# Optimization experiments

Measured on AMD Instinct MI355X. Metric: run time of the kernel, lower is better.

Reference implementation:

```python
import jax, jax.numpy as jnp
import numpy as np

HEADS = 4
CH = 64  # hidden_channels (per-head out channels)
N_INT = 50000
N_LANE = 400000
E_PO = 400000
E_ADJ = 200000


def setup_inputs() -> dict:
    key = jax.random.key(0)
    ks = iter(jax.random.split(key, 32))
    rn = lambda shape, s=0.1: jax.random.normal(next(ks), shape, dtype=jnp.float32) * s
    inp = {
        'x_int': rn((N_INT, 16), 1.0),
        'x_lane': rn((N_LANE, 12), 1.0),
        'h0': jnp.zeros((N_INT, CH), jnp.float32),
        'enc_int_W': rn((16, CH)), 'enc_int_b': jnp.zeros((CH,), jnp.float32),
        'enc_lane_W': rn((12, CH)), 'enc_lane_b': jnp.zeros((CH,), jnp.float32),
        'Wsrc_po': rn((CH, HEADS * CH)), 'Wdst_po': rn((CH, HEADS * CH)),
        'att_src_po': rn((HEADS, CH)), 'att_dst_po': rn((HEADS, CH)),
        'bias_po': jnp.zeros((HEADS * CH,), jnp.float32),
        'Wsrc_adj': rn((CH, HEADS * CH)), 'Wdst_adj': rn((CH, HEADS * CH)),
        'att_src_adj': rn((HEADS, CH)), 'att_dst_adj': rn((HEADS, CH)),
        'bias_adj': jnp.zeros((HEADS * CH,), jnp.float32),
        'gru_W_ih': rn((3 * CH, HEADS * CH)), 'gru_W_hh': rn((3 * CH, CH)),
        'gru_b_ih': jnp.zeros((3 * CH,), jnp.float32), 'gru_b_hh': jnp.zeros((3 * CH,), jnp.float32),
        'W_pi': rn((CH, 8)), 'b_pi': jnp.zeros((8,), jnp.float32),
        'W_v': rn((CH, 1)), 'b_v': jnp.zeros((1,), jnp.float32),
        'src_po': jax.random.randint(next(ks), (E_PO,), 0, N_LANE),
        'dst_po': jax.random.randint(next(ks), (E_PO,), 0, N_INT),
        'src_adj': jax.random.randint(next(ks), (E_ADJ,), 0, N_INT),
        'dst_adj': jax.random.randint(next(ks), (E_ADJ,), 0, N_INT),
    }
    return inp


def gat_conv(x_src, x_dst, src, dst, Wsrc, Wdst, a_src, a_dst, bias, n_dst):
    # PyG GATConv (bipartite, concat=True, no self loops), negative_slope=0.2
    hs = (x_src @ Wsrc).reshape(-1, HEADS, CH)  # [Ns,H,C]
    hd = (x_dst @ Wdst).reshape(-1, HEADS, CH)  # [Nd,H,C]
    a_s = jnp.einsum('nhc,hc->nh', hs, a_src)   # [Ns,H]
    a_d = jnp.einsum('nhc,hc->nh', hd, a_dst)   # [Nd,H]
    alpha = jax.nn.leaky_relu(a_s[src] + a_d[dst], 0.2)        # [E,H]
    amax = jax.ops.segment_max(alpha, dst, num_segments=n_dst)  # [Nd,H]
    ex = jnp.exp(alpha - amax[dst])
    den = jax.ops.segment_sum(ex, dst, num_segments=n_dst)
    w = ex / den[dst]                                           # [E,H] softmax per dst
    msg = hs[src] * w[:, :, None]                               # [E,H,C]
    out = jax.ops.segment_sum(msg, dst, num_segments=n_dst)     # [Nd,H,C]
    return out.reshape(n_dst, HEADS * CH) + bias


def gru_cell(x, h, W_ih, W_hh, b_ih, b_hh):
    gi = x @ W_ih.T + b_ih
    gh = h @ W_hh.T + b_hh
    i_r, i_z, i_n = jnp.split(gi, 3, axis=1)
    h_r, h_z, h_n = jnp.split(gh, 3, axis=1)
    r = jax.nn.sigmoid(i_r + h_r)
    z = jax.nn.sigmoid(i_z + h_z)
    n = jnp.tanh(i_n + r * h_n)
    return (1.0 - z) * n + z * h


def reference(x_int, x_lane, h0, enc_int_W, enc_int_b, enc_lane_W, enc_lane_b,
              Wsrc_po, Wdst_po, att_src_po, att_dst_po, bias_po,
              Wsrc_adj, Wdst_adj, att_src_adj, att_dst_adj, bias_adj,
              gru_W_ih, gru_W_hh, gru_b_ih, gru_b_hh,
              W_pi, b_pi, W_v, b_v,
              src_po, dst_po, src_adj, dst_adj):
    # per-type encoders + ReLU
    e_int = jax.nn.relu(x_int @ enc_int_W + enc_int_b)    # [N_int,CH]
    e_lane = jax.nn.relu(x_lane @ enc_lane_W + enc_lane_b)  # [N_lane,CH]
    # HeteroConv aggr='sum' over relations targeting 'intersection'
    o_po = gat_conv(e_lane, e_int, src_po, dst_po, Wsrc_po, Wdst_po,
                    att_src_po, att_dst_po, bias_po, N_INT)
    o_adj = gat_conv(e_int, e_int, src_adj, dst_adj, Wsrc_adj, Wdst_adj,
                     att_src_adj, att_dst_adj, bias_adj, N_INT)
    inter = jax.nn.relu(o_po + o_adj)  # dropout = identity (deterministic eval)
    h_new = gru_cell(inter, h0, gru_W_ih, gru_W_hh, gru_b_ih, gru_b_hh)
    logits = h_new @ W_pi + b_pi
    value = h_new @ W_v + b_v
    return logits, value, h_new
```

## Files before the change

kernel.cpp:

```cpp
#include <hip/hip_runtime.h>

#define NI 50000
#define NL 400000
#define EPO 400000
#define EADJ 200000

#define K1_ITER 8
#define K2_ITER 4
#define K1_ROWS (32*K1_ITER)
#define K2_ROWS (32*K2_ITER)
#define NLB ((NL + K1_ROWS - 1)/K1_ROWS)
#define NIB ((NI + K2_ROWS - 1)/K2_ROWS)
#define NHB ((EPO + EADJ + 255)/256)

typedef unsigned int u32;
typedef unsigned short u16;
typedef short bf16x8 __attribute__((ext_vector_type(8)));
typedef float f32x4 __attribute__((ext_vector_type(4)));

__device__ __forceinline__ float bf2f(u16 h){ return __uint_as_float(((u32)h)<<16); }
__device__ __forceinline__ u16 f2bf(float f){
  u32 u = __float_as_uint(f);
  u += 0x7FFFu + ((u>>16)&1u);
  return (u16)(u>>16);
}
__device__ __forceinline__ u32 pack2(float a, float b){
  return (u32)f2bf(a) | ((u32)f2bf(b)<<16);
}

__device__ __forceinline__ float b2_val(
    const float* __restrict__ W_ih, const float* __restrict__ W_hh, int m, int k)
{
  if(k < 256){ return (m<192) ? W_ih[m*256+k] : 0.f; }
  int kk = k-256;
  if(m<128) return W_hh[m*64+kk];
  if(m>=192) return W_hh[(m-64)*64+kk];
  return 0.f;
}

__global__ __launch_bounds__(256) void k0_prep(
    const float* __restrict__ Wsrc_po, const float* __restrict__ att_src_po,
    const float* __restrict__ Wdst_po, const float* __restrict__ att_dst_po,
    const float* __restrict__ Wsrc_adj, const float* __restrict__ att_src_adj,
    const float* __restrict__ Wdst_adj, const float* __restrict__ att_dst_adj,
    const float* __restrict__ W_ih, const float* __restrict__ W_hh,
    const float* __restrict__ bias_po, const float* __restrict__ bias_adj,
    const float* __restrict__ b_ih, const float* __restrict__ b_hh,
    float* __restrict__ v4, u16* __restrict__ WheadT, u16* __restrict__ B2F,
    float* __restrict__ bias_comb, float* __restrict__ bias2,
    int* __restrict__ cnt)
{
  const int T0 = 1024, T1 = 4*64*128, T2 = 10*16*64*8;
  const int TC = 2*NI;
  int total = T0 + T1 + T2 + 256 + 256 + TC;
  for(int t = blockIdx.x*256 + threadIdx.x; t < total; t += gridDim.x*256){
    if(t < T0){
      int which = t>>8, hc = t&255, h = hc>>6, c = hc&63;
      const float *W, *att;
      if(which==0){ W=Wsrc_po;  att=att_src_po; }
      else if(which==1){ W=Wdst_po;  att=att_dst_po; }
      else if(which==2){ W=Wsrc_adj; att=att_src_adj; }
      else { W=Wdst_adj; att=att_dst_adj; }
      float s=0.f;
      for(int j=0;j<64;j++) s += W[c*256 + h*64 + j]*att[h*64+j];
      v4[which*256 + hc] = s;
    } else if(t < T0 + T1){
      int i = t - T0; int h = i>>13, rem = i&8191, m = rem>>7, k = rem&127;
      float val = (k<64) ? Wsrc_po[k*256 + h*64 + m]
                         : Wsrc_adj[(k-64)*256 + h*64 + m];
      WheadT[i] = f2bf(val);
    } else if(t < T0 + T1 + T2){
      int i = t - (T0+T1);
      int j = i&7;
      int u4 = i>>3;
      int kstep = u4>>10, rem = u4&1023, tile = rem>>6, lane = rem&63;
      int col = tile*16 + (lane&15);
      int k = kstep*32 + (lane>>4)*8 + j;
      B2F[i] = f2bf(b2_val(W_ih, W_hh, col, k));
    } else if(t < T0 + T1 + T2 + 256){
      int m = t - (T0+T1+T2);
      bias_comb[m] = bias_po[m] + bias_adj[m];
    } else if(t < T0 + T1 + T2 + 512){
      int m = t - (T0+T1+T2+256);
      float v;
      if(m<128) v = b_ih[m] + b_hh[m];
      else if(m<192) v = b_ih[m];
      else v = b_hh[m-64];
      bias2[m] = v;
    } else {
      cnt[t - (T0+T1+T2+512)] = 0;
    }
  }
}

__global__ __launch_bounds__(256) void k_enc(
    const float* __restrict__ x_lane, const float* __restrict__ Wl, const float* __restrict__ bl,
    const float* __restrict__ x_int,  const float* __restrict__ Wi, const float* __restrict__ bi,
    const float* __restrict__ v_sp, const float* __restrict__ v_dp,
    const float* __restrict__ v_sa, const float* __restrict__ v_da,
    u16* __restrict__ e_lane, float* __restrict__ a_s_po,
    u16* __restrict__ e_int, float* __restrict__ a_dp, float* __restrict__ a_sa,
    float* __restrict__ a_da,
    const int* __restrict__ dst_po, const int* __restrict__ dst_adj,
    int* __restrict__ cnt)
{
  int t = threadIdx.x;
  int wv = t>>6, l = t&63;
  int g = l&7, m = l>>3;
  int blk = blockIdx.x;
  if(blk < NLB){
    float wreg[12][8], breg[8];
#pragma unroll
    for(int k=0;k<12;k++){
      float4 w0 = *(const float4*)(Wl + k*64 + g*8);
      float4 w1 = *(const float4*)(Wl + k*64 + g*8 + 4);
      wreg[k][0]=w0.x; wreg[k][1]=w0.y; wreg[k][2]=w0.z; wreg[k][3]=w0.w;
      wreg[k][4]=w1.x; wreg[k][5]=w1.y; wreg[k][6]=w1.z; wreg[k][7]=w1.w;
    }
    {
      float4 b0 = *(const float4*)(bl + g*8);
      float4 b1 = *(const float4*)(bl + g*8 + 4);
      breg[0]=b0.x; breg[1]=b0.y; breg[2]=b0.z; breg[3]=b0.w;
      breg[4]=b1.x; breg[5]=b1.y; breg[6]=b1.z; breg[7]=b1.w;
    }
    int rowbase = blk*K1_ROWS + wv*(8*K1_ITER) + m;
    float4 Aa={0,0,0,0}, Ab={0,0,0,0}, Ac={0,0,0,0};
    float4 Ba={0,0,0,0}, Bb={0,0,0,0}, Bc={0,0,0,0};
    if(rowbase < NL){
      const float4* xp = (const float4*)(x_lane + (size_t)rowbase*12);
      Aa = xp[0]; Ab = xp[1]; Ac = xp[2];
    }
    if(rowbase+8 < NL){
      const float4* xp = (const float4*)(x_lane + (size_t)(rowbase+8)*12);
      Ba = xp[0]; Bb = xp[1]; Bc = xp[2];
    }
#pragma unroll
    for(int it=0; it<K1_ITER; it++){
      int row = rowbase + it*8;
      float4 Ca={0,0,0,0}, Cb={0,0,0,0}, Cc={0,0,0,0};
      if(it+2 < K1_ITER && row+16 < NL){
        const float4* xp = (const float4*)(x_lane + (size_t)(row+16)*12);
        Ca = xp[0]; Cb = xp[1]; Cc = xp[2];
      }
      float xv[12];
      xv[0]=Aa.x; xv[1]=Aa.y; xv[2]=Aa.z; xv[3]=Aa.w;
      xv[4]=Ab.x; xv[5]=Ab.y; xv[6]=Ab.z; xv[7]=Ab.w;
      xv[8]=Ac.x; xv[9]=Ac.y; xv[10]=Ac.z; xv[11]=Ac.w;
      float acc[8];
#pragma unroll
      for(int j=0;j<8;j++) acc[j]=breg[j];
#pragma unroll
      for(int k=0;k<12;k++){
        float xk = xv[k];
#pragma unroll
        for(int j=0;j<8;j++) acc[j] += xk*wreg[k][j];
      }
      float e[8];
#pragma unroll
      for(int j=0;j<8;j++) e[j] = fmaxf(acc[j], 0.f);
      float as[4];
#pragma unroll
      for(int h=0;h<4;h++){
        float4 v0 = *(const float4*)(v_sp + h*64 + g*8);
        float4 v1 = *(const float4*)(v_sp + h*64 + g*8 + 4);
        as[h] = e[0]*v0.x + e[1]*v0.y + e[2]*v0.z + e[3]*v0.w
              + e[4]*v1.x + e[5]*v1.y + e[6]*v1.z + e[7]*v1.w;
      }
#pragma unroll
      for(int o=1;o<8;o<<=1){
#pragma unroll
        for(int h=0;h<4;h++) as[h] += __shfl_xor(as[h], o, 64);
      }
      if(row < NL){
        uint4 P;
        P.x = pack2(e[0],e[1]); P.y = pack2(e[2],e[3]);
        P.z = pack2(e[4],e[5]); P.w = pack2(e[6],e[7]);
        ((uint4*)e_lane)[(size_t)row*8 + g] = P;
        if(g==0){
          float4 A; A.x=as[0]; A.y=as[1]; A.z=as[2]; A.w=as[3];
          *(float4*)(a_s_po + (size_t)row*4) = A;
        }
      }
      Aa=Ba; Ab=Bb; Ac=Bc;
      Ba=Ca; Bb=Cb; Bc=Cc;
    }
  } else if(blk < NLB + NIB){
    int b2 = blk - NLB;
    float breg[8];
    {
      float4 b0 = *(const float4*)(bi + g*8);
      float4 b1 = *(const float4*)(bi + g*8 + 4);
      breg[0]=b0.x; breg[1]=b0.y; breg[2]=b0.z; breg[3]=b0.w;
      breg[4]=b1.x; breg[5]=b1.y; breg[6]=b1.z; breg[7]=b1.w;
    }
    int rowbase = b2*K2_ROWS + wv*(8*K2_ITER) + m;
#pragma unroll
    for(int it=0; it<K2_ITER; it++){
      int row = rowbase + it*8;
      float xv[16];
      if(row < NI){
        const float4* xp = (const float4*)(x_int + (size_t)row*16);
#pragma unroll
        for(int q=0;q<4;q++){
          float4 xq = xp[q];
          xv[q*4]=xq.x; xv[q*4+1]=xq.y; xv[q*4+2]=xq.z; xv[q*4+3]=xq.w;
        }
      } else {
#pragma unroll
        for(int k=0;k<16;k++) xv[k]=0.f;
      }
      float acc[8];
#pragma unroll
      for(int j=0;j<8;j++) acc[j]=breg[j];
#pragma unroll
      for(int k=0;k<16;k++){
        float4 w0 = *(const float4*)(Wi + k*64 + g*8);
        float4 w1 = *(const float4*)(Wi + k*64 + g*8 + 4);
        float xk = xv[k];
        acc[0] += xk*w0.x; acc[1] += xk*w0.y; acc[2] += xk*w0.z; acc[3] += xk*w0.w;
        acc[4] += xk*w1.x; acc[5] += xk*w1.y; acc[6] += xk*w1.z; acc[7] += xk*w1.w;
      }
      float e[8];
#pragma unroll
      for(int j=0;j<8;j++) e[j] = fmaxf(acc[j], 0.f);
      float ad[4], sa[4], da[4];
#pragma unroll
      for(int h=0;h<4;h++){
        float4 v0, v1;
        v0 = *(const float4*)(v_dp + h*64 + g*8); v1 = *(const float4*)(v_dp + h*64 + g*8 + 4);
        ad[h] = e[0]*v0.x + e[1]*v0.y + e[2]*v0.z + e[3]*v0.w
              + e[4]*v1.x + e[5]*v1.y + e[6]*v1.z + e[7]*v1.w;
        v0 = *(const float4*)(v_sa + h*64 + g*8); v1 = *(const float4*)(v_sa + h*64 + g*8 + 4);
        sa[h] = e[0]*v0.x + e[1]*v0.y + e[2]*v0.z + e[3]*v0.w
              + e[4]*v1.x + e[5]*v1.y + e[6]*v1.z + e[7]*v1.w;
        v0 = *(const float4*)(v_da + h*64 + g*8); v1 = *(const float4*)(v_da + h*64 + g*8 + 4);
        da[h] = e[0]*v0.x + e[1]*v0.y + e[2]*v0.z + e[3]*v0.w
              + e[4]*v1.x + e[5]*v1.y + e[6]*v1.z + e[7]*v1.w;
      }
#pragma unroll
      for(int o=1;o<8;o<<=1){
#pragma unroll
        for(int h=0;h<4;h++){
          ad[h] += __shfl_xor(ad[h], o, 64);
          sa[h] += __shfl_xor(sa[h], o, 64);
          da[h] += __shfl_xor(da[h], o, 64);
        }
      }
      if(row < NI){
        uint4 P;
        P.x = pack2(e[0],e[1]); P.y = pack2(e[2],e[3]);
        P.z = pack2(e[4],e[5]); P.w = pack2(e[6],e[7]);
        ((uint4*)e_int)[(size_t)row*8 + g] = P;
        if(g==0){
          float4 A;
          A.x=ad[0]; A.y=ad[1]; A.z=ad[2]; A.w=ad[3]; *(float4*)(a_dp + (size_t)row*4) = A;
          A.x=sa[0]; A.y=sa[1]; A.z=sa[2]; A.w=sa[3]; *(float4*)(a_sa + (size_t)row*4) = A;
          A.x=da[0]; A.y=da[1]; A.z=da[2]; A.w=da[3]; *(float4*)(a_da + (size_t)row*4) = A;
        }
      }
    }
  } else {
    int i = (blk - NLB - NIB)*256 + t;
    if(i < EPO) atomicAdd(&cnt[dst_po[i]], 1);
    else if(i < EPO+EADJ) atomicAdd(&cnt[NI + dst_adj[i-EPO]], 1);
  }
}

__global__ __launch_bounds__(1024) void k4a_scan(
    const int* __restrict__ cnt, int* __restrict__ offA, int* __restrict__ bsum)
{
  __shared__ int s[1024];
  int y = blockIdx.y;
  int i = blockIdx.x*1024 + threadIdx.x;
  int v = (i<NI) ? cnt[y*NI+i] : 0;
  s[threadIdx.x]=v;
  __syncthreads();
  for(int o=1;o<1024;o<<=1){
    int t = (threadIdx.x>=o) ? s[threadIdx.x-o] : 0;
    __syncthreads();
    s[threadIdx.x] += t;
    __syncthreads();
  }
  if(i<NI) offA[y*NI+i] = s[threadIdx.x]-v;
  if(threadIdx.x==1023) bsum[y*64+blockIdx.x] = s[1023];
}

__global__ __launch_bounds__(128) void k4b_scanb(int* __restrict__ bsum)
{
  int y = threadIdx.x>>6, lane = threadIdx.x&63;
  int v = (lane<49) ? bsum[y*64+lane] : 0;
  int orig = v;
#pragma unroll
  for(int o=1;o<64;o<<=1){
    int t = __shfl_up(v,o,64);
    if(lane>=o) v += t;
  }
  if(lane<49) bsum[y*64+lane] = v-orig;
}

__global__ __launch_bounds__(1024) void k4c_add(
    int* __restrict__ offA, int* __restrict__ cur, const int* __restrict__ bsum)
{
  int y = blockIdx.y;
  int i = blockIdx.x*1024 + threadIdx.x;
  if(i<NI){
    int o = offA[y*NI+i] + bsum[y*64+blockIdx.x];
    offA[y*NI+i]=o;
    cur[y*NI+i]=o;
  }
}

__global__ __launch_bounds__(256) void k5_scatter(
    const int* __restrict__ src_po, const int* __restrict__ dst_po,
    const int* __restrict__ src_adj, const int* __restrict__ dst_adj,
    const float* __restrict__ a_s_po, const float* __restrict__ a_d_po,
    const float* __restrict__ a_s_adj, const float* __restrict__ a_d_adj,
    int* __restrict__ cur, int* __restrict__ csr_po, int* __restrict__ csr_adj,
    float* __restrict__ pw_po, float* __restrict__ pw_adj)
{
  int i = blockIdx.x*256 + threadIdx.x;
  if(i < EPO){
    int s = src_po[i];
    int d = dst_po[i];
    int p = atomicAdd(&cur[d],1);
    csr_po[p] = s;
    float4 as = *(const float4*)(a_s_po + (size_t)s*4);
    float4 ad = *(const float4*)(a_d_po + (size_t)d*4);
    float4 pv;
    float x;
    x = as.x+ad.x; pv.x = __expf(x>0.f?x:0.2f*x);
    x = as.y+ad.y; pv.y = __expf(x>0.f?x:0.2f*x);
    x = as.z+ad.z; pv.z = __expf(x>0.f?x:0.2f*x);
    x = as.w+ad.w; pv.w = __expf(x>0.f?x:0.2f*x);
    *(float4*)(pw_po + (size_t)p*4) = pv;
  } else if(i < EPO+EADJ){
    int e = i-EPO;
    int s = src_adj[e];
    int d = dst_adj[e];
    int p = atomicAdd(&cur[NI+d],1);
    csr_adj[p] = s;
    float4 as = *(const float4*)(a_s_adj + (size_t)s*4);
    float4 ad = *(const float4*)(a_d_adj + (size_t)d*4);
    float4 pv;
    float x;
    x = as.x+ad.x; pv.x = __expf(x>0.f?x:0.2f*x);
    x = as.y+ad.y; pv.y = __expf(x>0.f?x:0.2f*x);
    x = as.z+ad.z; pv.z = __expf(x>0.f?x:0.2f*x);
    x = as.w+ad.w; pv.w = __expf(x>0.f?x:0.2f*x);
    *(float4*)(pw_adj + (size_t)p*4) = pv;
  }
}

__device__ __forceinline__ void agg_rel(
    int beg, int n, int lane,
    const int* __restrict__ csr, const float* __restrict__ pw,
    const u16* __restrict__ emat, u16* __restrict__ aggrow)
{
  float l0=0,l1=0,l2=0,l3=0;
  float c0=0,c1=0,c2=0,c3=0;
  for(int base=0;base<n;base+=64){
    int m = n-base; if(m>64) m=64;
    int sv_ = (lane<m) ? csr[beg+base+lane] : 0;
    int t2=0;
    for(; t2+1<m; t2+=2){
      int s0 = __shfl(sv_, t2, 64);
      int s1 = __shfl(sv_, t2+1, 64);
      float4 p0 = *(const float4*)(pw + (size_t)(beg+base+t2)*4);
      float4 p1 = *(const float4*)(pw + (size_t)(beg+base+t2+1)*4);
      float e0 = bf2f(emat[(size_t)s0*64+lane]);
      float e1 = bf2f(emat[(size_t)s1*64+lane]);
      c0 += p0.x*e0; c1 += p0.y*e0; c2 += p0.z*e0; c3 += p0.w*e0;
      l0 += p0.x;    l1 += p0.y;    l2 += p0.z;    l3 += p0.w;
      c0 += p1.x*e1; c1 += p1.y*e1; c2 += p1.z*e1; c3 += p1.w*e1;
      l0 += p1.x;    l1 += p1.y;    l2 += p1.z;    l3 += p1.w;
    }
    if(t2<m){
      int s0 = __shfl(sv_, t2, 64);
      float4 p0 = *(const float4*)(pw + (size_t)(beg+base+t2)*4);
      float e0 = bf2f(emat[(size_t)s0*64+lane]);
      c0 += p0.x*e0; c1 += p0.y*e0; c2 += p0.z*e0; c3 += p0.w*e0;
      l0 += p0.x;    l1 += p0.y;    l2 += p0.z;    l3 += p0.w;
    }
  }
  aggrow[lane]       = f2bf(n>0 ? c0/l0 : 0.f);
  aggrow[64+lane]    = f2bf(n>0 ? c1/l1 : 0.f);
  aggrow[128+lane]   = f2bf(n>0 ? c2/l2 : 0.f);
  aggrow[192+lane]   = f2bf(n>0 ? c3/l3 : 0.f);
}

__global__ __launch_bounds__(512) void k6_agg(
    const int* __restrict__ off, const int* __restrict__ cnt,
    const int* __restrict__ csr_po, const int* __restrict__ csr_adj,
    const float* __restrict__ pw_po, const float* __restrict__ pw_adj,
    const u16* __restrict__ e_lane, const u16* __restrict__ e_int,
    u16* __restrict__ agg)
{
  int wave=threadIdx.x>>6, lane=threadIdx.x&63;
  int d = blockIdx.x*4 + (wave&3);
  if(d>=NI) return;
  if(wave < 4)
    agg_rel(off[d],    cnt[d],    lane, csr_po,  pw_po,  e_lane, agg + (size_t)d*512);
  else
    agg_rel(off[NI+d], cnt[NI+d], lane, csr_adj, pw_adj, e_int,  agg + (size_t)d*512 + 256);
}

__global__ __launch_bounds__(256) void k8_fused(
    const u16* __restrict__ agg, const u16* __restrict__ WheadT,
    const float* __restrict__ bias_comb,
    const uint4* __restrict__ B2F, const float* __restrict__ bias2,
    const float* __restrict__ h0,
    const float* __restrict__ Wpi, const float* __restrict__ bpi,
    const float* __restrict__ Wv, const float* __restrict__ bvp,
    float* __restrict__ out)
{
  __shared__ u16 As[64][136];
  __shared__ u16 Bs[64][136];
  __shared__ u16 interT[64][264];
  int t=threadIdx.x, w=t>>6, lane=t&63;
  int r = lane&15, q = lane>>4;
  int row0 = blockIdx.x*64;

  for(int h=0;h<4;h++){
    const uint4* Bsrc = (const uint4*)(WheadT + (size_t)h*8192);
    uint4 bvr[4], avr[4];
#pragma unroll
    for(int it=0; it<4; it++){
      int idx = it*256 + t;
      bvr[it] = Bsrc[idx];
      int brow = idx>>4, u4 = idx&15;
      int grow = row0 + brow;
      uint4 v = {0,0,0,0};
      if(grow < NI){
        int co = (u4<8) ? (h*64 + u4*8) : (256 + h*64 + (u4-8)*8);
        v = *(const uint4*)(agg + (size_t)grow*512 + co);
      }
      avr[it] = v;
    }
    __syncthreads();
#pragma unroll
    for(int it=0; it<4; it++){
      int idx = it*256 + t;
      int brow = idx>>4, u4 = idx&15;
      *(uint4*)&Bs[brow][u4*8] = bvr[it];
      *(uint4*)&As[brow][u4*8] = avr[it];
    }
    __syncthreads();
    f32x4 acc0={0,0,0,0}, acc1={0,0,0,0}, acc2={0,0,0,0}, acc3={0,0,0,0};
#pragma unroll
    for(int ks=0; ks<4; ks++){
      bf16x8 af = *(const bf16x8*)&As[w*16 + r][q*8 + ks*32];
      bf16x8 b0 = *(const bf16x8*)&Bs[ 0 + r][q*8 + ks*32];
      bf16x8 b1 = *(const bf16x8*)&Bs[16 + r][q*8 + ks*32];
      bf16x8 b2 = *(const bf16x8*)&Bs[32 + r][q*8 + ks*32];
      bf16x8 b3 = *(const bf16x8*)&Bs[48 + r][q*8 + ks*32];
      acc0 = __builtin_amdgcn_mfma_f32_16x16x32_bf16(af,b0,acc0,0,0,0);
      acc1 = __builtin_amdgcn_mfma_f32_16x16x32_bf16(af,b1,acc1,0,0,0);
      acc2 = __builtin_amdgcn_mfma_f32_16x16x32_bf16(af,b2,acc2,0,0,0);
      acc3 = __builtin_amdgcn_mfma_f32_16x16x32_bf16(af,b3,acc3,0,0,0);
    }
    int crow = w*16 + q*4;
#pragma unroll
    for(int t2=0;t2<4;t2++){
      f32x4 a = (t2==0)?acc0 : (t2==1)?acc1 : (t2==2)?acc2 : acc3;
      int col = h*64 + t2*16 + r;
      float bcol = bias_comb[col];
#pragma unroll
      for(int rr=0;rr<4;rr++)
        interT[crow+rr][col] = f2bf(fmaxf(a[rr]+bcol, 0.f));
    }
  }
  __syncthreads();

  int arowl = w*16 + r;
  int arow  = row0 + arowl;
  int arc = arow < NI ? arow : NI-1;
  const float* h0r = h0 + (size_t)arc*64 + q*8;
  f32x4 acc[16];
#pragma unroll
  for(int i=0;i<16;i++) acc[i] = (f32x4){0,0,0,0};
#pragma unroll
  for(int ks=0; ks<10; ks++){
    bf16x8 af;
    if(ks < 8){
      af = *(const bf16x8*)&interT[arowl][ks*32 + q*8];
    } else {
      const float* hp = h0r + (ks-8)*32;
      float4 f0 = *(const float4*)(hp);
      float4 f1 = *(const float4*)(hp+4);
      uint4 P;
      P.x = pack2(f0.x,f0.y); P.y = pack2(f0.z,f0.w);
      P.z = pack2(f1.x,f1.y); P.w = pack2(f1.z,f1.w);
      *(uint4*)&af = P;
    }
    const uint4* bp = B2F + ks*1024 + lane;
#pragma unroll
    for(int tt=0;tt<16;tt++){
      uint4 bu = bp[tt*64];
      bf16x8 bf; *(uint4*)&bf = bu;
      acc[tt] = __builtin_amdgcn_mfma_f32_16x16x32_bf16(af, bf, acc[tt], 0,0,0);
    }
  }
  float pk[4][8];
  float pv[4];
#pragma unroll
  for(int rr=0;rr<4;rr++){
    pv[rr]=0.f;
#pragma unroll
    for(int j=0;j<8;j++) pk[rr][j]=0.f;
  }
  int rbase = row0 + w*16 + q*4;
#pragma unroll
  for(int t2=0;t2<4;t2++){
    int c = t2*16 + r;
    float b0 = bias2[c], b1 = bias2[64+c], b2 = bias2[128+c], b3 = bias2[192+c];
    float wp[8];
#pragma unroll
    for(int j=0;j<8;j++) wp[j] = Wpi[c*8+j];
    float wv = Wv[c];
#pragma unroll
    for(int rr=0;rr<4;rr++){
      int row = rbase + rr;
      float g0 = acc[t2][rr]    + b0;
      float g1 = acc[t2+4][rr]  + b1;
      float g2 = acc[t2+8][rr]  + b2;
      float g3 = acc[t2+12][rr] + b3;
      float h0v = (row < NI) ? h0[(size_t)row*64 + c] : 0.f;
      float rg = 1.f/(1.f+__expf(-g0));
      float zg = 1.f/(1.f+__expf(-g1));
      float e2 = __expf(2.f*(g2 + rg*g3));
      float ng = 1.f - 2.f/(e2+1.f);
      float h = (1.f-zg)*ng + zg*h0v;
      if(row < NI) out[450000 + (size_t)row*64 + c] = h;
#pragma unroll
      for(int j=0;j<8;j++) pk[rr][j] += h*wp[j];
      pv[rr] += h*wv;
    }
  }
#pragma unroll
  for(int o=1;o<16;o<<=1){
#pragma unroll
    for(int rr=0;rr<4;rr++){
#pragma unroll
      for(int j=0;j<8;j++) pk[rr][j] += __shfl_xor(pk[rr][j], o, 64);
      pv[rr] += __shfl_xor(pv[rr], o, 64);
    }
  }
  if(r==0){
#pragma unroll
    for(int rr=0;rr<4;rr++){
      int row = rbase + rr;
      if(row < NI){
#pragma unroll
        for(int j=0;j<8;j++) out[(size_t)row*8 + j] = pk[rr][j] + bpi[j];
        out[400000 + row] = pv[rr] + bvp[0];
      }
    }
  }
}

extern "C" void kernel_launch(void* const* d_in, const int* in_sizes, int n_in,
                              void* d_out, int out_size, void* d_ws, size_t ws_size,
                              hipStream_t stream) {
  const float* x_int      = (const float*)d_in[0];
  const float* x_lane     = (const float*)d_in[1];
  const float* h0         = (const float*)d_in[2];
  const float* enc_int_W  = (const float*)d_in[3];
  const float* enc_int_b  = (const float*)d_in[4];
  const float* enc_lane_W = (const float*)d_in[5];
  const float* enc_lane_b = (const float*)d_in[6];
  const float* Wsrc_po    = (const float*)d_in[7];
  const float* Wdst_po    = (const float*)d_in[8];
  const float* att_src_po = (const float*)d_in[9];
  const float* att_dst_po = (const float*)d_in[10];
  const float* bias_po    = (const float*)d_in[11];
  const float* Wsrc_adj   = (const float*)d_in[12];
  const float* Wdst_adj   = (const float*)d_in[13];
  const float* att_src_adj= (const float*)d_in[14];
  const float* att_dst_adj= (const float*)d_in[15];
  const float* bias_adj   = (const float*)d_in[16];
  const float* gru_W_ih   = (const float*)d_in[17];
  const float* gru_W_hh   = (const float*)d_in[18];
  const float* gru_b_ih   = (const float*)d_in[19];
  const float* gru_b_hh   = (const float*)d_in[20];
  const float* W_pi       = (const float*)d_in[21];
  const float* b_pi       = (const float*)d_in[22];
  const float* W_v        = (const float*)d_in[23];
  const float* b_v        = (const float*)d_in[24];
  const int* src_po  = (const int*)d_in[25];
  const int* dst_po  = (const int*)d_in[26];
  const int* src_adj = (const int*)d_in[27];
  const int* dst_adj = (const int*)d_in[28];
  float* out = (float*)d_out;

  char* w = (char*)d_ws;
  size_t ofs = 0;
  auto alloc = [&](size_t bytes)->char*{
    char* p = w + ofs;
    ofs = (ofs + bytes + 255) & ~(size_t)255;
    return p;
  };
  u16*  e_lane   = (u16*)alloc((size_t)NL*64*2);
  u16*  e_int    = (u16*)alloc((size_t)NI*64*2);
  float* a_s_po  = (float*)alloc((size_t)NL*4*4);
  float* a_d_po  = (float*)alloc((size_t)NI*4*4);
  float* a_s_adj = (float*)alloc((size_t)NI*4*4);
  float* a_d_adj = (float*)alloc((size_t)NI*4*4);
  int*  cnt      = (int*)alloc((size_t)2*NI*4);
  int*  offA     = (int*)alloc((size_t)2*NI*4);
  int*  cur      = (int*)alloc((size_t)2*NI*4);
  int*  csr_po   = (int*)alloc((size_t)EPO*4);
  int*  csr_adj  = (int*)alloc((size_t)EADJ*4);
  float* pw_po   = (float*)alloc((size_t)EPO*4*4);
  float* pw_adj  = (float*)alloc((size_t)EADJ*4*4);
  int*  bsum     = (int*)alloc(2*64*4);
  u16*  agg      = (u16*)alloc((size_t)NI*512*2);
  u16*  WheadT   = (u16*)alloc(4*64*128*2);
  u16*  B2F      = (u16*)alloc(10*16*64*8*2);
  float* v4      = (float*)alloc(4*256*4);
  float* bias_comb = (float*)alloc(256*4);
  float* bias2   = (float*)alloc(256*4);
  (void)ws_size; (void)n_in; (void)in_sizes; (void)out_size;

  k0_prep<<<256, 256, 0, stream>>>(
      Wsrc_po, att_src_po, Wdst_po, att_dst_po,
      Wsrc_adj, att_src_adj, Wdst_adj, att_dst_adj,
      gru_W_ih, gru_W_hh, bias_po, bias_adj, gru_b_ih, gru_b_hh,
      v4, WheadT, B2F, bias_comb, bias2, cnt);
  k_enc<<<NLB+NIB+NHB, 256, 0, stream>>>(
      x_lane, enc_lane_W, enc_lane_b,
      x_int, enc_int_W, enc_int_b,
      v4 + 0, v4 + 256, v4 + 512, v4 + 768,
      e_lane, a_s_po, e_int, a_d_po, a_s_adj, a_d_adj,
      dst_po, dst_adj, cnt);
  k4a_scan<<<dim3(49,2), 1024, 0, stream>>>(cnt, offA, bsum);
  k4b_scanb<<<1, 128, 0, stream>>>(bsum);
  k4c_add<<<dim3(49,2), 1024, 0, stream>>>(offA, cur, bsum);
  k5_scatter<<<(EPO+EADJ+255)/256, 256, 0, stream>>>(src_po, dst_po, src_adj, dst_adj,
      a_s_po, a_d_po, a_s_adj, a_d_adj,
      cur, csr_po, csr_adj, pw_po, pw_adj);
  k6_agg<<<(NI+3)/4, 512, 0, stream>>>(offA, cnt, csr_po, csr_adj,
      pw_po, pw_adj, e_lane, e_int, agg);
  k8_fused<<<(NI+63)/64, 256, 0, stream>>>(agg, WheadT, bias_comb,
      (const uint4*)B2F, bias2, h0, W_pi, b_pi, W_v, b_v, out);
}
```

Baseline: 369.7 us.

## Prepack head weights into MFMA fragment layout, drop LDS staging, unroll gather by four

```diff
diff --git a/kernel.cpp b/kernel.cpp
--- a/kernel.cpp
+++ b/kernel.cpp
@@ -46,11 +46,11 @@
     const float* __restrict__ W_ih, const float* __restrict__ W_hh,
     const float* __restrict__ bias_po, const float* __restrict__ bias_adj,
     const float* __restrict__ b_ih, const float* __restrict__ b_hh,
-    float* __restrict__ v4, u16* __restrict__ WheadT, u16* __restrict__ B2F,
+    float* __restrict__ v4, u16* __restrict__ WheadF, u16* __restrict__ B2F,
     float* __restrict__ bias_comb, float* __restrict__ bias2,
     int* __restrict__ cnt)
 {
-  const int T0 = 1024, T1 = 4*64*128, T2 = 10*16*64*8;
+  const int T0 = 1024, T1 = 4*4*4*64*8, T2 = 10*16*64*8;
   const int TC = 2*NI;
   int total = T0 + T1 + T2 + 256 + 256 + TC;
   for(int t = blockIdx.x*256 + threadIdx.x; t < total; t += gridDim.x*256){
@@ -65,10 +65,18 @@
       for(int j=0;j<64;j++) s += W[c*256 + h*64 + j]*att[h*64+j];
       v4[which*256 + hc] = s;
     } else if(t < T0 + T1){
-      int i = t - T0; int h = i>>13, rem = i&8191, m = rem>>7, k = rem&127;
-      float val = (k<64) ? Wsrc_po[k*256 + h*64 + m]
-                         : Wsrc_adj[(k-64)*256 + h*64 + m];
-      WheadT[i] = f2bf(val);
+      int i = t - T0;
+      int j = i&7;
+      int u4 = i>>3;
+      int lane = u4&63;
+      int rem = u4>>6;
+      int ct = rem&3, kt = (rem>>2)&3, h = rem>>4;
+      int r = lane&15, qb = lane>>4;
+      int kp = kt*32 + qb*8 + j;
+      int n = ct*16 + r;
+      float val = (kp<64) ? Wsrc_po[kp*256 + h*64 + n]
+                          : Wsrc_adj[(kp-64)*256 + h*64 + n];
+      WheadF[i] = f2bf(val);
     } else if(t < T0 + T1 + T2){
       int i = t - (T0+T1);
       int j = i&7;
@@ -362,19 +370,29 @@
     int m = n-base; if(m>64) m=64;
     int sv_ = (lane<m) ? csr[beg+base+lane] : 0;
     int t2=0;
-    for(; t2+1<m; t2+=2){
-      int s0 = __shfl(sv_, t2, 64);
+    for(; t2+3<m; t2+=4){
+      int s0 = __shfl(sv_, t2,   64);
       int s1 = __shfl(sv_, t2+1, 64);
-      float4 p0 = *(const float4*)(pw + (size_t)(beg+base+t2)*4);
+      int s2 = __shfl(sv_, t2+2, 64);
+      int s3 = __shfl(sv_, t2+3, 64);
+      float4 p0 = *(const float4*)(pw + (size_t)(beg+base+t2  )*4);
       float4 p1 = *(const float4*)(pw + (size_t)(beg+base+t2+1)*4);
+      float4 p2 = *(const float4*)(pw + (size_t)(beg+base+t2+2)*4);
+      float4 p3 = *(const float4*)(pw + (size_t)(beg+base+t2+3)*4);
       float e0 = bf2f(emat[(size_t)s0*64+lane]);
       float e1 = bf2f(emat[(size_t)s1*64+lane]);
+      float e2 = bf2f(emat[(size_t)s2*64+lane]);
+      float e3 = bf2f(emat[(size_t)s3*64+lane]);
       c0 += p0.x*e0; c1 += p0.y*e0; c2 += p0.z*e0; c3 += p0.w*e0;
       l0 += p0.x;    l1 += p0.y;    l2 += p0.z;    l3 += p0.w;
       c0 += p1.x*e1; c1 += p1.y*e1; c2 += p1.z*e1; c3 += p1.w*e1;
       l0 += p1.x;    l1 += p1.y;    l2 += p1.z;    l3 += p1.w;
-    }
-    if(t2<m){
+      c0 += p2.x*e2; c1 += p2.y*e2; c2 += p2.z*e2; c3 += p2.w*e2;
+      l0 += p2.x;    l1 += p2.y;    l2 += p2.z;    l3 += p2.w;
+      c0 += p3.x*e3; c1 += p3.y*e3; c2 += p3.z*e3; c3 += p3.w*e3;
+      l0 += p3.x;    l1 += p3.y;    l2 += p3.z;    l3 += p3.w;
+    }
+    for(; t2<m; t2++){
       int s0 = __shfl(sv_, t2, 64);
       float4 p0 = *(const float4*)(pw + (size_t)(beg+base+t2)*4);
       float e0 = bf2f(emat[(size_t)s0*64+lane]);
@@ -405,7 +423,7 @@
 }
 
 __global__ __launch_bounds__(256) void k8_fused(
-    const u16* __restrict__ agg, const u16* __restrict__ WheadT,
+    const u16* __restrict__ agg, const uint4* __restrict__ WheadF,
     const float* __restrict__ bias_comb,
     const uint4* __restrict__ B2F, const float* __restrict__ bias2,
     const float* __restrict__ h0,
@@ -413,60 +431,38 @@
     const float* __restrict__ Wv, const float* __restrict__ bvp,
     float* __restrict__ out)
 {
-  __shared__ u16 As[64][136];
-  __shared__ u16 Bs[64][136];
   __shared__ u16 interT[64][264];
   int t=threadIdx.x, w=t>>6, lane=t&63;
   int r = lane&15, q = lane>>4;
   int row0 = blockIdx.x*64;
-
-  for(int h=0;h<4;h++){
-    const uint4* Bsrc = (const uint4*)(WheadT + (size_t)h*8192);
-    uint4 bvr[4], avr[4];
-#pragma unroll
-    for(int it=0; it<4; it++){
-      int idx = it*256 + t;
-      bvr[it] = Bsrc[idx];
-      int brow = idx>>4, u4 = idx&15;
-      int grow = row0 + brow;
-      uint4 v = {0,0,0,0};
-      if(grow < NI){
-        int co = (u4<8) ? (h*64 + u4*8) : (256 + h*64 + (u4-8)*8);
-        v = *(const uint4*)(agg + (size_t)grow*512 + co);
-      }
-      avr[it] = v;
-    }
-    __syncthreads();
-#pragma unroll
-    for(int it=0; it<4; it++){
-      int idx = it*256 + t;
-      int brow = idx>>4, u4 = idx&15;
-      *(uint4*)&Bs[brow][u4*8] = bvr[it];
-      *(uint4*)&As[brow][u4*8] = avr[it];
-    }
-    __syncthreads();
-    f32x4 acc0={0,0,0,0}, acc1={0,0,0,0}, acc2={0,0,0,0}, acc3={0,0,0,0};
-#pragma unroll
-    for(int ks=0; ks<4; ks++){
-      bf16x8 af = *(const bf16x8*)&As[w*16 + r][q*8 + ks*32];
-      bf16x8 b0 = *(const bf16x8*)&Bs[ 0 + r][q*8 + ks*32];
-      bf16x8 b1 = *(const bf16x8*)&Bs[16 + r][q*8 + ks*32];
-      bf16x8 b2 = *(const bf16x8*)&Bs[32 + r][q*8 + ks*32];
-      bf16x8 b3 = *(const bf16x8*)&Bs[48 + r][q*8 + ks*32];
-      acc0 = __builtin_amdgcn_mfma_f32_16x16x32_bf16(af,b0,acc0,0,0,0);
-      acc1 = __builtin_amdgcn_mfma_f32_16x16x32_bf16(af,b1,acc1,0,0,0);
-      acc2 = __builtin_amdgcn_mfma_f32_16x16x32_bf16(af,b2,acc2,0,0,0);
-      acc3 = __builtin_amdgcn_mfma_f32_16x16x32_bf16(af,b3,acc3,0,0,0);
-    }
-    int crow = w*16 + q*4;
-#pragma unroll
-    for(int t2=0;t2<4;t2++){
-      f32x4 a = (t2==0)?acc0 : (t2==1)?acc1 : (t2==2)?acc2 : acc3;
-      int col = h*64 + t2*16 + r;
+  int h = w;
+
+  const uint4* BF = WheadF + (size_t)h*16*64;
+#pragma unroll
+  for(int rt=0; rt<4; rt++){
+    int row = row0 + rt*16 + r;
+    int arc = row < NI ? row : NI-1;
+    const u16* arow_p = agg + (size_t)arc*512;
+    bf16x8 af[4];
+#pragma unroll
+    for(int kt=0; kt<4; kt++){
+      int colbase = (kt<2) ? (h*64 + kt*32) : (256 + h*64 + (kt-2)*32);
+      af[kt] = *(const bf16x8*)(arow_p + colbase + q*8);
+    }
+#pragma unroll
+    for(int ct=0; ct<4; ct++){
+      f32x4 facc = {0,0,0,0};
+#pragma unroll
+      for(int kt=0; kt<4; kt++){
+        uint4 bu = BF[(kt*4 + ct)*64 + lane];
+        bf16x8 bfr; *(uint4*)&bfr = bu;
+        facc = __builtin_amdgcn_mfma_f32_16x16x32_bf16(af[kt], bfr, facc, 0,0,0);
+      }
+      int col = h*64 + ct*16 + r;
       float bcol = bias_comb[col];
 #pragma unroll
-      for(int rr=0;rr<4;rr++)
-        interT[crow+rr][col] = f2bf(fmaxf(a[rr]+bcol, 0.f));
+      for(int rr=0; rr<4; rr++)
+        interT[rt*16 + q*4 + rr][col] = f2bf(fmaxf(facc[rr]+bcol, 0.f));
     }
   }
   __syncthreads();
@@ -496,8 +492,8 @@
 #pragma unroll
     for(int tt=0;tt<16;tt++){
       uint4 bu = bp[tt*64];
-      bf16x8 bf; *(uint4*)&bf = bu;
-      acc[tt] = __builtin_amdgcn_mfma_f32_16x16x32_bf16(af, bf, acc[tt], 0,0,0);
+      bf16x8 bfr; *(uint4*)&bfr = bu;
+      acc[tt] = __builtin_amdgcn_mfma_f32_16x16x32_bf16(af, bfr, acc[tt], 0,0,0);
     }
   }
   float pk[4][8];
@@ -529,11 +525,11 @@
       float zg = 1.f/(1.f+__expf(-g1));
       float e2 = __expf(2.f*(g2 + rg*g3));
       float ng = 1.f - 2.f/(e2+1.f);
-      float h = (1.f-zg)*ng + zg*h0v;
-      if(row < NI) out[450000 + (size_t)row*64 + c] = h;
-#pragma unroll
-      for(int j=0;j<8;j++) pk[rr][j] += h*wp[j];
-      pv[rr] += h*wv;
+      float hh = (1.f-zg)*ng + zg*h0v;
+      if(row < NI) out[450000 + (size_t)row*64 + c] = hh;
+#pragma unroll
+      for(int j=0;j<8;j++) pk[rr][j] += hh*wp[j];
+      pv[rr] += hh*wv;
     }
   }
 #pragma unroll
@@ -614,7 +610,7 @@
   float* pw_adj  = (float*)alloc((size_t)EADJ*4*4);
   int*  bsum     = (int*)alloc(2*64*4);
   u16*  agg      = (u16*)alloc((size_t)NI*512*2);
-  u16*  WheadT   = (u16*)alloc(4*64*128*2);
+  u16*  WheadF   = (u16*)alloc(4*4*4*64*8*2);
   u16*  B2F      = (u16*)alloc(10*16*64*8*2);
   float* v4      = (float*)alloc(4*256*4);
   float* bias_comb = (float*)alloc(256*4);
@@ -625,7 +621,7 @@
       Wsrc_po, att_src_po, Wdst_po, att_dst_po,
       Wsrc_adj, att_src_adj, Wdst_adj, att_dst_adj,
       gru_W_ih, gru_W_hh, bias_po, bias_adj, gru_b_ih, gru_b_hh,
-      v4, WheadT, B2F, bias_comb, bias2, cnt);
+      v4, WheadF, B2F, bias_comb, bias2, cnt);
   k_enc<<<NLB+NIB+NHB, 256, 0, stream>>>(
       x_lane, enc_lane_W, enc_lane_b,
       x_int, enc_int_W, enc_int_b,
@@ -640,6 +636,6 @@
       cur, csr_po, csr_adj, pw_po, pw_adj);
   k6_agg<<<(NI+3)/4, 512, 0, stream>>>(offA, cnt, csr_po, csr_adj,
       pw_po, pw_adj, e_lane, e_int, agg);
-  k8_fused<<<(NI+63)/64, 256, 0, stream>>>(agg, WheadT, bias_comb,
+  k8_fused<<<(NI+63)/64, 256, 0, stream>>>(agg, (const uint4*)WheadF, bias_comb,
       (const uint4*)B2F, bias2, h0, W_pi, b_pi, W_v, b_v, out);
 }
```

After: 404.7 us. +9.5%, slower.
